# Kernel optimization log

Measured on AMD Instinct MI355X. Metric: run time of the kernel, lower is better.

The kernel has to match this reference:

```python
import jax, jax.numpy as jnp
import numpy as np

B, N, C = 1, 4096, 1024
H = 16
HD = C // H  # head_dim = 64
SCALE = HD ** -0.5


def setup_inputs() -> dict:
    key = jax.random.key(0)
    k1, k2, k3, k4, k5 = jax.random.split(key, 5)
    x1 = jax.random.normal(k1, (B, N, C), dtype=jnp.float32)
    x2 = jax.random.normal(k2, (B, N, C), dtype=jnp.float32)
    # qkv: Linear(dim, 2*all_head_dim), bias=False. Stored as (in, out) for x @ W.
    W_qkv = jax.random.normal(k3, (C, 2 * H * HD), dtype=jnp.float32) * (C ** -0.5)
    # proj: Linear(all_head_dim, dim) with bias
    W_proj = jax.random.normal(k4, (H * HD, C), dtype=jnp.float32) * ((H * HD) ** -0.5)
    b_proj = jax.random.normal(k5, (C,), dtype=jnp.float32) * 0.01
    return {"x1": x1, "x2": x2, "W_qkv": W_qkv, "W_proj": W_proj, "b_proj": b_proj}


def reference(x1, x2, W_qkv, W_proj, b_proj):
    b, n, c = x1.shape
    # qk projection: (B,N,2*H*HD) -> (2,B,H,N,HD)
    qkv = (x1 @ W_qkv).reshape(b, n, 2, H, HD).transpose(2, 0, 3, 1, 4)
    q, k = qkv[0], qkv[1]  # (B,H,N,HD)
    # V2: reshape (N,1,H,HD) then permute -> (1,H,N,HD); valid since B==1
    v = x2.reshape(n, 1, H, HD).transpose(1, 2, 0, 3)
    attn = jax.nn.softmax(jnp.einsum('bhnd,bhmd->bhnm', q * SCALE, k), axis=-1)
    out = jnp.einsum('bhnm,bhmd->bhnd', attn, v)  # broadcasts v over batch
    out = out.transpose(0, 2, 1, 3).reshape(b, n, H * HD)
    return out @ W_proj + b_proj
```

## Files before the change

### kernel.cpp

```cpp
#include <hip/hip_runtime.h>

typedef unsigned short u16;
typedef unsigned int u32;

#define HNUM 16
#define NSEQ 4096
#define CDIM 1024
#define SCALE 0.125f
#define LOG2E 1.4426950408889634f

using bf16x8 = __attribute__((ext_vector_type(8))) __bf16;
using f32x4  = __attribute__((ext_vector_type(4))) float;

__device__ __forceinline__ u16 f2bf(float f) {
  union { float f; u32 u; } v; v.f = f;
  u32 u = v.u;
  return (u16)((u + 0x7fffu + ((u >> 16) & 1u)) >> 16);
}
__device__ __forceinline__ float fexp2(float x) { return __builtin_amdgcn_exp2f(x); }

__device__ __forceinline__ f32x4 mfma16(bf16x8 a, bf16x8 b, f32x4 c) {
  return __builtin_amdgcn_mfma_f32_16x16x32_bf16(a, b, c, 0, 0, 0);
}

__device__ __forceinline__ u32 pack2(float a, float b) {
  union { float f; u32 u; } A, B;
  A.f = a; B.f = b;
  return __builtin_amdgcn_perm(B.u + 0x8000u, A.u + 0x8000u, 0x07060302u);
}

__device__ __forceinline__ void g2l16(const void* g, void* l) {
  __builtin_amdgcn_global_load_lds(
      (const __attribute__((address_space(1))) unsigned int*)(unsigned long long)g,
      (__attribute__((address_space(3))) unsigned int*)(unsigned int)(unsigned long long)l,
      16, 0, 0);
}

__global__ __launch_bounds__(256) void cvt_k(const float* __restrict__ in,
                                             u16* __restrict__ out) {
  const int i = (blockIdx.x * 256 + threadIdx.x) * 8;
  const float4 f0 = *(const float4*)(in + i);
  const float4 f1 = *(const float4*)(in + i + 4);
  u32 d[4] = {pack2(f0.x, f0.y), pack2(f0.z, f0.w),
              pack2(f1.x, f1.y), pack2(f1.z, f1.w)};
  *(bf16x8*)(out + i) = *(bf16x8*)d;
}

__global__ __launch_bounds__(256) void cvtT_k(const float* __restrict__ in,
                                              u16* __restrict__ out, int R, int C,
                                              int scaleRows, float scale) {
  __shared__ u16 t[64][65];
  const int tid = threadIdx.x;
  const int r0 = blockIdx.y * 64, c0 = blockIdx.x * 64;
  const int tr = tid >> 2, tc = (tid & 3) * 16;
  const float s = (c0 < scaleRows) ? scale : 1.0f;
  const float* src = in + (r0 + tr) * C + c0 + tc;
#pragma unroll
  for (int i = 0; i < 16; ++i) t[tr][tc + i] = f2bf(src[i] * s);
  __syncthreads();
  u16* dst = out + (c0 + tr) * R + r0 + tc;
#pragma unroll
  for (int i = 0; i < 16; ++i) dst[i] = t[tc + i][tr];
}

__global__ __launch_bounds__(256) void gemm1_k(const u16* __restrict__ A,
                                               const u16* __restrict__ Bt,
                                               u16* __restrict__ C,
                                               int M, int N, int K) {
  __shared__ __align__(16) u16 As[128 * 64];
  __shared__ __align__(16) u16 Bs[128 * 64];
  const int tid = threadIdx.x;
  const int wave = tid >> 6, lane = tid & 63;
  const int quad = lane >> 4, l16 = lane & 15;
  const int m0 = blockIdx.y * 128, n0 = blockIdx.x * 128;
  const int wm = (wave >> 1) * 64, wn = (wave & 1) * 64;
  const int lrow = lane >> 3, lc8 = (lane & 7) * 8;

  f32x4 acc[4][4] = {};
  for (int k0 = 0; k0 < K; k0 += 64) {
#pragma unroll
    for (int c = 0; c < 4; ++c) {
      const int cw = wave * 4 + c;
      g2l16(A  + (m0 + cw * 8 + lrow) * K + k0 + lc8, (char*)As + cw * 1024);
      g2l16(Bt + (n0 + cw * 8 + lrow) * K + k0 + lc8, (char*)Bs + cw * 1024);
    }
    __syncthreads();
#pragma unroll
    for (int ks = 0; ks < 2; ++ks) {
      bf16x8 a[4], b[4];
#pragma unroll
      for (int mt = 0; mt < 4; ++mt)
        a[mt] = *(const bf16x8*)(As + (wm + mt * 16 + l16) * 64 + ks * 32 + quad * 8);
#pragma unroll
      for (int nt = 0; nt < 4; ++nt)
        b[nt] = *(const bf16x8*)(Bs + (wn + nt * 16 + l16) * 64 + ks * 32 + quad * 8);
#pragma unroll
      for (int mt = 0; mt < 4; ++mt)
#pragma unroll
        for (int nt = 0; nt < 4; ++nt)
          acc[mt][nt] = mfma16(a[mt], b[nt], acc[mt][nt]);
    }
    __syncthreads();
  }
#pragma unroll
  for (int mt = 0; mt < 4; ++mt)
#pragma unroll
    for (int nt = 0; nt < 4; ++nt)
#pragma unroll
      for (int r = 0; r < 4; ++r)
        C[(m0 + wm + mt * 16 + quad * 4 + r) * N + n0 + wn + nt * 16 + l16] =
            f2bf(acc[mt][nt][r]);
}

__global__ __launch_bounds__(256) void gemm2_k(const u16* __restrict__ A,
                                               const u16* __restrict__ Bt,
                                               float* __restrict__ C,
                                               const float* __restrict__ bias,
                                               int M, int N, int K) {
  __shared__ __align__(16) u16 As[128 * 64];
  __shared__ __align__(16) u16 Bs[128 * 64];
  const int tid = threadIdx.x;
  const int wave = tid >> 6, lane = tid & 63;
  const int quad = lane >> 4, l16 = lane & 15;
  const int m0 = blockIdx.y * 128, n0 = blockIdx.x * 128;
  const int wm = (wave >> 1) * 64, wn = (wave & 1) * 64;
  const int lrow = lane >> 3, lc8 = (lane & 7) * 8;

  f32x4 acc[4][4] = {};
  for (int k0 = 0; k0 < K; k0 += 64) {
#pragma unroll
    for (int c = 0; c < 4; ++c) {
      const int cw = wave * 4 + c;
      g2l16(A  + (m0 + cw * 8 + lrow) * K + k0 + lc8, (char*)As + cw * 1024);
      g2l16(Bt + (n0 + cw * 8 + lrow) * K + k0 + lc8, (char*)Bs + cw * 1024);
    }
    __syncthreads();
#pragma unroll
    for (int ks = 0; ks < 2; ++ks) {
      bf16x8 a[4], b[4];
#pragma unroll
      for (int mt = 0; mt < 4; ++mt)
        a[mt] = *(const bf16x8*)(As + (wm + mt * 16 + l16) * 64 + ks * 32 + quad * 8);
#pragma unroll
      for (int nt = 0; nt < 4; ++nt)
        b[nt] = *(const bf16x8*)(Bs + (wn + nt * 16 + l16) * 64 + ks * 32 + quad * 8);
#pragma unroll
      for (int mt = 0; mt < 4; ++mt)
#pragma unroll
        for (int nt = 0; nt < 4; ++nt)
          acc[mt][nt] = mfma16(a[mt], b[nt], acc[mt][nt]);
    }
    __syncthreads();
  }
#pragma unroll
  for (int mt = 0; mt < 4; ++mt)
#pragma unroll
    for (int nt = 0; nt < 4; ++nt)
#pragma unroll
      for (int r = 0; r < 4; ++r) {
        const int col = n0 + wn + nt * 16 + l16;
        C[(m0 + wm + mt * 16 + quad * 4 + r) * N + col] = acc[mt][nt][r] + bias[col];
      }
}

__global__ __launch_bounds__(128) void attn_k(const u16* __restrict__ QK,
                                              const u16* __restrict__ Vt,
                                              u16* __restrict__ O) {
  __shared__ __align__(16) u16 Ks[64 * 64];
  __shared__ __align__(16) u16 Vs[64 * 64];
  __shared__ __align__(16) u16 Ps[2][32 * 64];
  const int tid = threadIdx.x;
  const int wave = tid >> 6, lane = tid & 63;
  const int quad = lane >> 4, l16 = lane & 15;
  const int head = blockIdx.y;
  const int qb = blockIdx.x * 64 + wave * 32;
  const int lrow = lane >> 3;
  const int lc8 = ((lane & 7) ^ lrow) * 8;
  const int swz = (quad ^ (l16 & 7)) * 8;

  bf16x8 qf[2][2];
#pragma unroll
  for (int mt = 0; mt < 2; ++mt)
#pragma unroll
    for (int ks = 0; ks < 2; ++ks)
      qf[mt][ks] = *(const bf16x8*)(QK + (qb + mt * 16 + l16) * 2048 + head * 64 +
                                    ks * 32 + quad * 8);

  f32x4 o[2][4] = {};
  float lsum[2] = {};
  u16* Pw = Ps[wave];

  for (int kt0 = 0; kt0 < NSEQ; kt0 += 64) {
#pragma unroll
    for (int c = 0; c < 4; ++c) {
      const int cw = wave * 4 + c;
      const int row = cw * 8 + lrow;
      g2l16(QK + (kt0 + row) * 2048 + CDIM + head * 64 + lc8, (char*)Ks + cw * 1024);
      g2l16(Vt + (head * 64 + row) * NSEQ + kt0 + lc8,        (char*)Vs + cw * 1024);
    }
    __syncthreads();

    f32x4 s[2][4] = {};
#pragma unroll
    for (int ks = 0; ks < 2; ++ks)
#pragma unroll
      for (int nt = 0; nt < 4; ++nt) {
        const bf16x8 kf =
            *(const bf16x8*)(Ks + (nt * 16 + l16) * 64 + (swz ^ (ks * 32)));
#pragma unroll
        for (int mt = 0; mt < 2; ++mt)
          s[mt][nt] = mfma16(kf, qf[mt][ks], s[mt][nt]);
      }

#pragma unroll
    for (int mt = 0; mt < 2; ++mt)
#pragma unroll
      for (int nt = 0; nt < 4; ++nt) {
        const float p0 = fexp2(s[mt][nt][0]);
        const float p1 = fexp2(s[mt][nt][1]);
        const float p2 = fexp2(s[mt][nt][2]);
        const float p3 = fexp2(s[mt][nt][3]);
        lsum[mt] += (p0 + p1) + (p2 + p3);
        u32 d01 = pack2(p0, p1), d23 = pack2(p2, p3);
        const int col8 = (nt * 2 + (quad >> 1)) ^ (l16 & 7);
        u32* dst = (u32*)(Pw + (mt * 16 + l16) * 64 + col8 * 8 + (quad & 1) * 4);
        dst[0] = d01; dst[1] = d23;
      }

#pragma unroll
    for (int ks = 0; ks < 2; ++ks) {
      bf16x8 pf[2];
#pragma unroll
      for (int mt = 0; mt < 2; ++mt)
        pf[mt] = *(const bf16x8*)(Pw + (mt * 16 + l16) * 64 + (swz ^ (ks * 32)));
#pragma unroll
      for (int dt = 0; dt < 4; ++dt) {
        const bf16x8 vf =
            *(const bf16x8*)(Vs + (dt * 16 + l16) * 64 + (swz ^ (ks * 32)));
#pragma unroll
        for (int mt = 0; mt < 2; ++mt)
          o[mt][dt] = mfma16(pf[mt], vf, o[mt][dt]);
      }
    }
    __syncthreads();
  }

  float linv[2];
#pragma unroll
  for (int mt = 0; mt < 2; ++mt) {
    float v = lsum[mt];
    v += __shfl_xor(v, 16, 64);
    v += __shfl_xor(v, 32, 64);
    linv[mt] = 1.0f / v;
  }
#pragma unroll
  for (int mt = 0; mt < 2; ++mt)
#pragma unroll
    for (int r = 0; r < 4; ++r) {
      const float lv = __shfl(linv[mt], (lane & 48) | (quad * 4 + r), 64);
#pragma unroll
      for (int dt = 0; dt < 4; ++dt)
        O[(qb + mt * 16 + quad * 4 + r) * CDIM + head * 64 + dt * 16 + l16] =
            f2bf(o[mt][dt][r] * lv);
    }
}

extern "C" void kernel_launch(void* const* d_in, const int* in_sizes, int n_in,
                              void* d_out, int out_size, void* d_ws, size_t ws_size,
                              hipStream_t stream) {
  const float* x1    = (const float*)d_in[0];
  const float* x2    = (const float*)d_in[1];
  const float* Wqkv  = (const float*)d_in[2];
  const float* Wproj = (const float*)d_in[3];
  const float* bproj = (const float*)d_in[4];
  float* out = (float*)d_out;

  char* ws = (char*)d_ws;
  u16* QK  = (u16*)(ws);
  u16* Vt  = (u16*)(ws + 16u * 1024 * 1024);
  u16* Obf = (u16*)(ws + 24u * 1024 * 1024);
  u16* WpT = (u16*)(ws + 32u * 1024 * 1024);
  u16* WqT = (u16*)(ws + 34u * 1024 * 1024);
  u16* x1b = (u16*)(ws + 38u * 1024 * 1024);

  const float cfac = SCALE * LOG2E;

  cvt_k<<<dim3(4096 * 1024 / 2048), 256, 0, stream>>>(x1, x1b);
  cvtT_k<<<dim3(2048 / 64, 1024 / 64), 256, 0, stream>>>(Wqkv, WqT, 1024, 2048,
                                                         1024, cfac);
  cvtT_k<<<dim3(1024 / 64, 1024 / 64), 256, 0, stream>>>(Wproj, WpT, 1024, 1024,
                                                         0, 1.0f);
  cvtT_k<<<dim3(1024 / 64, 4096 / 64), 256, 0, stream>>>(x2, Vt, 4096, 1024,
                                                         0, 1.0f);

  gemm1_k<<<dim3(2048 / 128, 4096 / 128), 256, 0, stream>>>(x1b, WqT, QK,
                                                            4096, 2048, 1024);
  attn_k<<<dim3(4096 / 64, HNUM), 128, 0, stream>>>(QK, Vt, Obf);
  gemm2_k<<<dim3(1024 / 128, 4096 / 128), 256, 0, stream>>>(Obf, WpT, out, bproj,
                                                            4096, 1024, 1024);
}
```

Baseline: 266.0 us.

## Double-buffer K/V tiles in attention to overlap loads with MFMA compute

The attention kernel now keeps two LDS buffers each for the K and V tiles. It issues the global-to-LDS loads for the next 64-key tile right after the barrier, before computing on the current tile, so memory latency can overlap with the QK^T, softmax and PV work. This replaces two barriers per iteration with one. Per-chunk load pointers are precomputed and advanced incrementally. The cost is doubled K/V LDS use, which may reduce how many blocks fit per CU.

```diff
diff --git a/kernel.cpp b/kernel.cpp
--- a/kernel.cpp
+++ b/kernel.cpp
@@ -166,8 +166,8 @@
 __global__ __launch_bounds__(128) void attn_k(const u16* __restrict__ QK,
                                               const u16* __restrict__ Vt,
                                               u16* __restrict__ O) {
-  __shared__ __align__(16) u16 Ks[64 * 64];
-  __shared__ __align__(16) u16 Vs[64 * 64];
+  __shared__ __align__(16) u16 Ks[2][64 * 64];
+  __shared__ __align__(16) u16 Vs[2][64 * 64];
   __shared__ __align__(16) u16 Ps[2][32 * 64];
   const int tid = threadIdx.x;
   const int wave = tid >> 6, lane = tid & 63;
@@ -178,6 +178,15 @@
   const int lc8 = ((lane & 7) ^ lrow) * 8;
   const int swz = (quad ^ (l16 & 7)) * 8;
 
+  const u16* kp[4];
+  const u16* vp[4];
+#pragma unroll
+  for (int c = 0; c < 4; ++c) {
+    const int row = (wave * 4 + c) * 8 + lrow;
+    kp[c] = QK + row * 2048 + CDIM + head * 64 + lc8;
+    vp[c] = Vt + (head * 64 + row) * NSEQ + lc8;
+  }
+
   bf16x8 qf[2][2];
 #pragma unroll
   for (int mt = 0; mt < 2; ++mt)
@@ -190,15 +199,32 @@
   float lsum[2] = {};
   u16* Pw = Ps[wave];
 
-  for (int kt0 = 0; kt0 < NSEQ; kt0 += 64) {
-#pragma unroll
-    for (int c = 0; c < 4; ++c) {
-      const int cw = wave * 4 + c;
-      const int row = cw * 8 + lrow;
-      g2l16(QK + (kt0 + row) * 2048 + CDIM + head * 64 + lc8, (char*)Ks + cw * 1024);
-      g2l16(Vt + (head * 64 + row) * NSEQ + kt0 + lc8,        (char*)Vs + cw * 1024);
-    }
-    __syncthreads();
+#pragma unroll
+  for (int c = 0; c < 4; ++c) {
+    const int cw = wave * 4 + c;
+    g2l16(kp[c], (char*)Ks[0] + cw * 1024);
+    g2l16(vp[c], (char*)Vs[0] + cw * 1024);
+    kp[c] += 64 * 2048;
+    vp[c] += 64;
+  }
+
+  for (int kt = 0; kt < NSEQ / 64; ++kt) {
+    const int cur = kt & 1;
+    __syncthreads();
+
+    if (kt < NSEQ / 64 - 1) {
+#pragma unroll
+      for (int c = 0; c < 4; ++c) {
+        const int cw = wave * 4 + c;
+        g2l16(kp[c], (char*)Ks[1 - cur] + cw * 1024);
+        g2l16(vp[c], (char*)Vs[1 - cur] + cw * 1024);
+        kp[c] += 64 * 2048;
+        vp[c] += 64;
+      }
+    }
+
+    const u16* Kc = Ks[cur];
+    const u16* Vc = Vs[cur];
 
     f32x4 s[2][4] = {};
 #pragma unroll
@@ -206,7 +232,7 @@
 #pragma unroll
       for (int nt = 0; nt < 4; ++nt) {
         const bf16x8 kf =
-            *(const bf16x8*)(Ks + (nt * 16 + l16) * 64 + (swz ^ (ks * 32)));
+            *(const bf16x8*)(Kc + (nt * 16 + l16) * 64 + (swz ^ (ks * 32)));
 #pragma unroll
         for (int mt = 0; mt < 2; ++mt)
           s[mt][nt] = mfma16(kf, qf[mt][ks], s[mt][nt]);
@@ -236,13 +262,12 @@
 #pragma unroll
       for (int dt = 0; dt < 4; ++dt) {
         const bf16x8 vf =
-            *(const bf16x8*)(Vs + (dt * 16 + l16) * 64 + (swz ^ (ks * 32)));
+            *(const bf16x8*)(Vc + (dt * 16 + l16) * 64 + (swz ^ (ks * 32)));
 #pragma unroll
         for (int mt = 0; mt < 2; ++mt)
           o[mt][dt] = mfma16(pf[mt], vf, o[mt][dt]);
       }
     }
-    __syncthreads();
   }
 
   float linv[2];
```

After: 255.4 us. 4.0% less time.
